# Optimization experiments

Hardware: AMD Instinct MI355X
Metric: run time of the kernel (lower is better)

The kernel has to match this reference:

```python
import jax, jax.numpy as jnp
import numpy as np
import math

N = 8192
D = 512

def setup_inputs() -> dict:
    key = jax.random.key(0)
    k1, k2, k3, k4, k5 = jax.random.split(key, 5)
    x = jax.random.normal(k1, (N, D), dtype=jnp.float32)
    mask = jax.random.randint(k2, (N, N), 0, 2) == 1
    s = 1.0 / math.sqrt(D)
    Wq = jax.random.normal(k3, (D, D), dtype=jnp.float32) * s
    Wk = jax.random.normal(k4, (D, D), dtype=jnp.float32) * s
    Wv = jax.random.normal(k5, (D, D), dtype=jnp.float32) * s
    return {"x": x, "mask": mask, "Wq": Wq, "Wk": Wk, "Wv": Wv}

def reference(x, mask, Wq, Wk, Wv):
    d_model = x.shape[-1]
    # torch nn.Linear: y = x @ W^T
    Q = x @ Wq.T
    K = x @ Wk.T
    V = x @ Wv.T
    scores = (Q @ K.T) / jnp.sqrt(jnp.asarray(d_model, x.dtype))  # [N, N]
    scores = jnp.where(mask, jnp.asarray(-1e9, x.dtype), scores)
    # manual stable softmax, matching the original op sequence
    scores = jnp.exp(scores - jnp.max(scores, axis=1, keepdims=True))
    attn = scores / jnp.sum(scores, axis=-1, keepdims=True)
    cntx = attn @ V
    return (cntx, attn)
```

## Files before the change

kernel.cpp:

```cpp
#include <hip/hip_runtime.h>

#define NTOK 8192
#define DMODEL 512

typedef _Float16 f16;
typedef _Float16 f16x4 __attribute__((ext_vector_type(4)));
typedef _Float16 f16x8 __attribute__((ext_vector_type(8)));
typedef float f32x4 __attribute__((ext_vector_type(4)));

__device__ __forceinline__ void async_ld16(const void* g, void* l) {
  __builtin_amdgcn_global_load_lds((const __attribute__((address_space(1))) void*)g,
                                   (__attribute__((address_space(3))) void*)l, 16, 0, 0);
}

__global__ void pack_f16(const float* __restrict__ s, f16* __restrict__ d, int n) {
  int i = (blockIdx.x * 256 + threadIdx.x) * 4;
  if (i >= n) return;
  float4 v = *(const float4*)(s + i);
  f16x4 h; h.x = (f16)v.x; h.y = (f16)v.y; h.z = (f16)v.z; h.w = (f16)v.w;
  *(f16x4*)(d + i) = h;
}

__global__ __launch_bounds__(256) void transpose_f16(const f16* __restrict__ src,
                                                     f16* __restrict__ dst) {
  __shared__ f16 T[64][72];
  int t = threadIdx.x;
  int tok0 = blockIdx.x * 64, d0 = blockIdx.y * 64;
#pragma unroll
  for (int i = 0; i < 2; ++i) {
    int row = (t >> 3) + i * 32;
    int col = (t & 7) * 8;
    f16x8 v = *(const f16x8*)(src + (size_t)(tok0 + row) * DMODEL + d0 + col);
    *(f16x8*)(&T[row][col]) = v;
  }
  __syncthreads();
#pragma unroll
  for (int i = 0; i < 2; ++i) {
    int od = (t >> 3) + i * 32;
    int ot = (t & 7) * 8;
    f16x8 v;
#pragma unroll
    for (int j = 0; j < 8; ++j) v[j] = T[ot + j][od];
    *(f16x8*)(dst + (size_t)(d0 + od) * NTOK + tok0 + ot) = v;
  }
}

__device__ __forceinline__ void stage128x32(const f16* G, int r0, int k0, int rs,
                                            f16* lds, int t) {
  int wv = t >> 6;
  const f16* g0 = G + (size_t)(r0 + (t >> 2)) * rs + k0 + (t & 3) * 8;
  async_ld16(g0, (char*)lds + wv * 1024);
  const f16* g1 = g0 + (size_t)64 * rs;
  async_ld16(g1, (char*)lds + 4096 + wv * 1024);
}

__global__ __launch_bounds__(256) void qkv_gemm(const f16* __restrict__ X,
                                                const f16* __restrict__ Wall,
                                                f16* __restrict__ Out) {
  __shared__ f16 As[128 * 32];
  __shared__ f16 Bs[128 * 32];
  int t = threadIdx.x;
  int z = blockIdx.z;
  const f16* B = Wall + (size_t)z * DMODEL * DMODEL;
  f16* C = Out + (size_t)z * NTOK * DMODEL;
  int m0 = blockIdx.y * 128, n0 = blockIdx.x * 128;
  int lane = t & 63, wv = t >> 6, quad = lane >> 4, l15 = lane & 15;
  int m_off = (wv & 1) * 64, n_off = (wv >> 1) * 64;
  f32x4 acc[4][4] = {};
  for (int kt = 0; kt < DMODEL; kt += 32) {
    __syncthreads();
    stage128x32(X, m0, kt, DMODEL, As, t);
    stage128x32(B, n0, kt, DMODEL, Bs, t);
    __syncthreads();
    f16x8 af[4], bf[4];
    const f16x8* Av = (const f16x8*)As;
    const f16x8* Bv = (const f16x8*)Bs;
#pragma unroll
    for (int mt = 0; mt < 4; ++mt) af[mt] = Av[(m_off + mt * 16 + l15) * 4 + quad];
#pragma unroll
    for (int nt = 0; nt < 4; ++nt) bf[nt] = Bv[(n_off + nt * 16 + l15) * 4 + quad];
#pragma unroll
    for (int mt = 0; mt < 4; ++mt)
#pragma unroll
      for (int nt = 0; nt < 4; ++nt)
        acc[mt][nt] = __builtin_amdgcn_mfma_f32_16x16x32_f16(af[mt], bf[nt], acc[mt][nt], 0, 0, 0);
  }
#pragma unroll
  for (int mt = 0; mt < 4; ++mt)
#pragma unroll
    for (int nt = 0; nt < 4; ++nt)
#pragma unroll
      for (int r = 0; r < 4; ++r) {
        int row = m0 + m_off + mt * 16 + quad * 4 + r;
        int col = n0 + n_off + nt * 16 + l15;
        C[(size_t)row * DMODEL + col] = (f16)acc[mt][nt][r];
      }
}

__global__ __launch_bounds__(256) void scores_kernel(const f16* __restrict__ Q,
                                                     const f16* __restrict__ Kh,
                                                     const int* __restrict__ mask,
                                                     float* __restrict__ E,
                                                     float* __restrict__ rowsum) {
  __shared__ f16 As[128 * 32];
  __shared__ f16 Bs[128 * 32];
  int t = threadIdx.x;
  int m0 = blockIdx.y * 128, n0 = blockIdx.x * 128;
  int lane = t & 63, wv = t >> 6, quad = lane >> 4, l15 = lane & 15;
  int m_off = (wv & 1) * 64, n_off = (wv >> 1) * 64;
  f32x4 acc[4][4] = {};
  for (int kt = 0; kt < DMODEL; kt += 32) {
    __syncthreads();
    stage128x32(Q, m0, kt, DMODEL, As, t);
    stage128x32(Kh, n0, kt, DMODEL, Bs, t);
    __syncthreads();
    f16x8 af[4], bf[4];
    const f16x8* Av = (const f16x8*)As;
    const f16x8* Bv = (const f16x8*)Bs;
#pragma unroll
    for (int mt = 0; mt < 4; ++mt) af[mt] = Av[(m_off + mt * 16 + l15) * 4 + quad];
#pragma unroll
    for (int nt = 0; nt < 4; ++nt) bf[nt] = Bv[(n_off + nt * 16 + l15) * 4 + quad];
#pragma unroll
    for (int mt = 0; mt < 4; ++mt)
#pragma unroll
      for (int nt = 0; nt < 4; ++nt)
        acc[mt][nt] = __builtin_amdgcn_mfma_f32_16x16x32_f16(af[mt], bf[nt], acc[mt][nt], 0, 0, 0);
  }
  const float scale = 0.044194173824159216f;
#pragma unroll
  for (int mt = 0; mt < 4; ++mt)
#pragma unroll
    for (int r = 0; r < 4; ++r) {
      int row = m0 + m_off + mt * 16 + quad * 4 + r;
      float rs = 0.f;
#pragma unroll
      for (int nt = 0; nt < 4; ++nt) {
        int col = n0 + n_off + nt * 16 + l15;
        size_t idx = (size_t)row * NTOK + col;
        float s = acc[mt][nt][r] * scale;
        float e = mask[idx] ? 0.f : __expf(s);
        E[idx] = e;
        rs += e;
      }
      rs += __shfl_xor(rs, 1);
      rs += __shfl_xor(rs, 2);
      rs += __shfl_xor(rs, 4);
      rs += __shfl_xor(rs, 8);
      if (l15 == 0) atomicAdd(&rowsum[row], rs);
    }
}

__global__ __launch_bounds__(512, 2) void norm_ev(float* __restrict__ E,
                                                  const float* __restrict__ rowsum,
                                                  const f16* __restrict__ Vt,
                                                  float* __restrict__ cntx) {
  __shared__ f16 Es[128 * 32];
  __shared__ f16 Vs[512 * 32];
  int t = threadIdx.x;
  int r0 = blockIdx.x * 128;
  int k0 = blockIdx.y * 2048;
  int lane = t & 63, wv = t >> 6, quad = lane >> 4, l15 = lane & 15;
  int m_off = (wv & 1) * 64, n_off = (wv >> 1) * 128;
  int srow = t >> 3, scol = (t & 7) * 4;
  float rinv0 = 1.f / rowsum[r0 + srow];
  float rinv1 = 1.f / rowsum[r0 + srow + 64];
  f32x4 acc[4][8] = {};
  for (int kt = k0; kt < k0 + 2048; kt += 32) {
    __syncthreads();
    {
      size_t g = (size_t)(r0 + srow) * NTOK + kt + scol;
      float4 v = *(const float4*)(E + g);
      v.x *= rinv0; v.y *= rinv0; v.z *= rinv0; v.w *= rinv0;
      *(float4*)(E + g) = v;
      f16x4 h; h.x = (f16)v.x; h.y = (f16)v.y; h.z = (f16)v.z; h.w = (f16)v.w;
      *(f16x4*)(Es + srow * 32 + scol) = h;
      size_t g2 = g + (size_t)64 * NTOK;
      float4 v2 = *(const float4*)(E + g2);
      v2.x *= rinv1; v2.y *= rinv1; v2.z *= rinv1; v2.w *= rinv1;
      *(float4*)(E + g2) = v2;
      f16x4 h2; h2.x = (f16)v2.x; h2.y = (f16)v2.y; h2.z = (f16)v2.z; h2.w = (f16)v2.w;
      *(f16x4*)(Es + (srow + 64) * 32 + scol) = h2;
    }
#pragma unroll
    for (int i = 0; i < 4; ++i) {
      const f16* g = Vt + (size_t)((i * 512 + t) >> 2) * NTOK + kt + (t & 3) * 8;
      async_ld16(g, (char*)Vs + i * 8192 + wv * 1024);
    }
    __syncthreads();
    f16x8 af[4], bf[8];
    const f16x8* Ev = (const f16x8*)Es;
    const f16x8* Vv = (const f16x8*)Vs;
#pragma unroll
    for (int mt = 0; mt < 4; ++mt) af[mt] = Ev[(m_off + mt * 16 + l15) * 4 + quad];
#pragma unroll
    for (int nt = 0; nt < 8; ++nt) bf[nt] = Vv[(n_off + nt * 16 + l15) * 4 + quad];
#pragma unroll
    for (int mt = 0; mt < 4; ++mt)
#pragma unroll
      for (int nt = 0; nt < 8; ++nt)
        acc[mt][nt] = __builtin_amdgcn_mfma_f32_16x16x32_f16(af[mt], bf[nt], acc[mt][nt], 0, 0, 0);
  }
#pragma unroll
  for (int mt = 0; mt < 4; ++mt)
#pragma unroll
    for (int nt = 0; nt < 8; ++nt)
#pragma unroll
      for (int r = 0; r < 4; ++r) {
        int row = r0 + m_off + mt * 16 + quad * 4 + r;
        int col = n_off + nt * 16 + l15;
        atomicAdd(&cntx[(size_t)row * DMODEL + col], acc[mt][nt][r]);
      }
}

extern "C" void kernel_launch(void* const* d_in, const int* in_sizes, int n_in,
                              void* d_out, int out_size, void* d_ws, size_t ws_size,
                              hipStream_t stream) {
  const float* x  = (const float*)d_in[0];
  const int* mask = (const int*)d_in[1];
  const float* Wq = (const float*)d_in[2];
  const float* Wk = (const float*)d_in[3];
  const float* Wv = (const float*)d_in[4];
  float* cntx = (float*)d_out;
  float* attn = (float*)d_out + (size_t)NTOK * DMODEL;

  f16* xh = (f16*)d_ws;
  f16* Wh = xh + (size_t)NTOK * DMODEL;
  f16* QKV = Wh + (size_t)3 * DMODEL * DMODEL;
  f16* Qh = QKV;
  f16* Kh = QKV + (size_t)NTOK * DMODEL;
  f16* Vh = QKV + (size_t)2 * NTOK * DMODEL;
  f16* Vt = QKV + (size_t)3 * NTOK * DMODEL;
  float* rowsum = (float*)(Vt + (size_t)NTOK * DMODEL);

  hipMemsetAsync(cntx, 0, (size_t)NTOK * DMODEL * sizeof(float), stream);
  hipMemsetAsync(rowsum, 0, NTOK * sizeof(float), stream);

  pack_f16<<<dim3(NTOK * DMODEL / 1024), 256, 0, stream>>>(x, xh, NTOK * DMODEL);
  pack_f16<<<dim3(DMODEL * DMODEL / 1024), 256, 0, stream>>>(Wq, Wh, DMODEL * DMODEL);
  pack_f16<<<dim3(DMODEL * DMODEL / 1024), 256, 0, stream>>>(Wk, Wh + DMODEL * DMODEL, DMODEL * DMODEL);
  pack_f16<<<dim3(DMODEL * DMODEL / 1024), 256, 0, stream>>>(Wv, Wh + 2 * DMODEL * DMODEL, DMODEL * DMODEL);

  qkv_gemm<<<dim3(DMODEL / 128, NTOK / 128, 3), 256, 0, stream>>>(xh, Wh, QKV);
  transpose_f16<<<dim3(NTOK / 64, DMODEL / 64), 256, 0, stream>>>(Vh, Vt);
  scores_kernel<<<dim3(NTOK / 128, NTOK / 128), 256, 0, stream>>>(Qh, Kh, mask, attn, rowsum);
  norm_ev<<<dim3(NTOK / 128, 4), 512, 0, stream>>>(attn, rowsum, Vt, cntx);
}
```

Baseline: 791.2 us.

## Bit-pack mask, store fp16 exp scores in-place, defer normalization to epilogues

Packs the int mask into 64-bit ballot words, which replaces the 256MB int read in the scores kernel. The scores kernel now writes unnormalized fp16 exponentials through a swizzled LDS tile into the attn buffer, using a 2x row stride. The PV kernel loads those fp16 values asynchronously and applies 1/rowsum in its epilogue, so it no longer does the fp32 read-modify-write of attn. A final in-place expand kernel converts the fp16 values back to normalized fp32 attn by walking backwards. The GEMM K-step also goes from 32 to 64. The cntx output buffer serves as scratch for the mask bits, and the attn values pass through fp16, which costs precision.

```diff
diff --git a/kernel.cpp b/kernel.cpp
--- a/kernel.cpp
+++ b/kernel.cpp
@@ -2,11 +2,14 @@
 
 #define NTOK 8192
 #define DMODEL 512
+#define NWORDS 128
+#define ESTRIDE (2 * NTOK)
 
 typedef _Float16 f16;
 typedef _Float16 f16x4 __attribute__((ext_vector_type(4)));
 typedef _Float16 f16x8 __attribute__((ext_vector_type(8)));
 typedef float f32x4 __attribute__((ext_vector_type(4)));
+typedef unsigned long long u64;
 
 __device__ __forceinline__ void async_ld16(const void* g, void* l) {
   __builtin_amdgcn_global_load_lds((const __attribute__((address_space(1))) void*)g,
@@ -21,6 +24,19 @@
   *(f16x4*)(d + i) = h;
 }
 
+__global__ __launch_bounds__(256) void pack_mask(const int* __restrict__ mask,
+                                                 u64* __restrict__ bits) {
+  int wave = (blockIdx.x * 256 + threadIdx.x) >> 6;
+  int lane = threadIdx.x & 63;
+  size_t W0 = (size_t)wave * 8;
+#pragma unroll
+  for (int i = 0; i < 8; ++i) {
+    int m = mask[(W0 + i) * 64 + lane];
+    u64 b = __ballot(m != 0);
+    if (lane == 0) bits[W0 + i] = b;
+  }
+}
+
 __global__ __launch_bounds__(256) void transpose_f16(const f16* __restrict__ src,
                                                      f16* __restrict__ dst) {
   __shared__ f16 T[64][72];
@@ -45,20 +61,48 @@
   }
 }
 
-__device__ __forceinline__ void stage128x32(const f16* G, int r0, int k0, int rs,
+__device__ __forceinline__ void stage128x64(const f16* G, int r0, int k0, int rs,
                                             f16* lds, int t) {
   int wv = t >> 6;
-  const f16* g0 = G + (size_t)(r0 + (t >> 2)) * rs + k0 + (t & 3) * 8;
-  async_ld16(g0, (char*)lds + wv * 1024);
-  const f16* g1 = g0 + (size_t)64 * rs;
-  async_ld16(g1, (char*)lds + 4096 + wv * 1024);
+  const f16* g = G + (size_t)(r0 + (t >> 3)) * rs + k0 + (t & 7) * 8;
+#pragma unroll
+  for (int i = 0; i < 4; ++i)
+    async_ld16(g + (size_t)i * 32 * rs, (char*)lds + i * 4096 + wv * 1024);
+}
+
+template <int RS>
+__device__ __forceinline__ void gemm128(const f16* A, const f16* B, int m0, int n0,
+                                        f16* As, f16* Bs, int t, f32x4 (&acc)[4][4]) {
+  int lane = t & 63, wv = t >> 6, quad = lane >> 4, l15 = lane & 15;
+  int m_off = (wv & 1) * 64, n_off = (wv >> 1) * 64;
+  for (int kt = 0; kt < RS; kt += 64) {
+    __syncthreads();
+    stage128x64(A, m0, kt, RS, As, t);
+    stage128x64(B, n0, kt, RS, Bs, t);
+    __syncthreads();
+#pragma unroll
+    for (int ks = 0; ks < 2; ++ks) {
+      f16x8 af[4], bf[4];
+#pragma unroll
+      for (int mt = 0; mt < 4; ++mt)
+        af[mt] = *(const f16x8*)(As + (m_off + mt * 16 + l15) * 64 + ks * 32 + quad * 8);
+#pragma unroll
+      for (int nt = 0; nt < 4; ++nt)
+        bf[nt] = *(const f16x8*)(Bs + (n_off + nt * 16 + l15) * 64 + ks * 32 + quad * 8);
+#pragma unroll
+      for (int mt = 0; mt < 4; ++mt)
+#pragma unroll
+        for (int nt = 0; nt < 4; ++nt)
+          acc[mt][nt] = __builtin_amdgcn_mfma_f32_16x16x32_f16(af[mt], bf[nt], acc[mt][nt], 0, 0, 0);
+    }
+  }
 }
 
 __global__ __launch_bounds__(256) void qkv_gemm(const f16* __restrict__ X,
                                                 const f16* __restrict__ Wall,
                                                 f16* __restrict__ Out) {
-  __shared__ f16 As[128 * 32];
-  __shared__ f16 Bs[128 * 32];
+  __shared__ f16 As[128 * 64];
+  __shared__ f16 Bs[128 * 64];
   int t = threadIdx.x;
   int z = blockIdx.z;
   const f16* B = Wall + (size_t)z * DMODEL * DMODEL;
@@ -67,24 +111,7 @@
   int lane = t & 63, wv = t >> 6, quad = lane >> 4, l15 = lane & 15;
   int m_off = (wv & 1) * 64, n_off = (wv >> 1) * 64;
   f32x4 acc[4][4] = {};
-  for (int kt = 0; kt < DMODEL; kt += 32) {
-    __syncthreads();
-    stage128x32(X, m0, kt, DMODEL, As, t);
-    stage128x32(B, n0, kt, DMODEL, Bs, t);
-    __syncthreads();
-    f16x8 af[4], bf[4];
-    const f16x8* Av = (const f16x8*)As;
-    const f16x8* Bv = (const f16x8*)Bs;
-#pragma unroll
-    for (int mt = 0; mt < 4; ++mt) af[mt] = Av[(m_off + mt * 16 + l15) * 4 + quad];
-#pragma unroll
-    for (int nt = 0; nt < 4; ++nt) bf[nt] = Bv[(n_off + nt * 16 + l15) * 4 + quad];
-#pragma unroll
-    for (int mt = 0; mt < 4; ++mt)
-#pragma unroll
-      for (int nt = 0; nt < 4; ++nt)
-        acc[mt][nt] = __builtin_amdgcn_mfma_f32_16x16x32_f16(af[mt], bf[nt], acc[mt][nt], 0, 0, 0);
-  }
+  gemm128<DMODEL>(X, B, m0, n0, As, Bs, t, acc);
 #pragma unroll
   for (int mt = 0; mt < 4; ++mt)
 #pragma unroll
@@ -97,51 +124,38 @@
       }
 }
 
-__global__ __launch_bounds__(256) void scores_kernel(const f16* __restrict__ Q,
-                                                     const f16* __restrict__ Kh,
-                                                     const int* __restrict__ mask,
-                                                     float* __restrict__ E,
-                                                     float* __restrict__ rowsum) {
-  __shared__ f16 As[128 * 32];
-  __shared__ f16 Bs[128 * 32];
+__global__ __launch_bounds__(256) void scores2(const f16* __restrict__ Q,
+                                               const f16* __restrict__ Kh,
+                                               const u64* __restrict__ bits,
+                                               f16* __restrict__ Eh,
+                                               float* __restrict__ rowsum) {
+  __shared__ f16 SM[128 * 128];
+  f16* As = SM;
+  f16* Bs = SM + 128 * 64;
   int t = threadIdx.x;
   int m0 = blockIdx.y * 128, n0 = blockIdx.x * 128;
   int lane = t & 63, wv = t >> 6, quad = lane >> 4, l15 = lane & 15;
   int m_off = (wv & 1) * 64, n_off = (wv >> 1) * 64;
   f32x4 acc[4][4] = {};
-  for (int kt = 0; kt < DMODEL; kt += 32) {
-    __syncthreads();
-    stage128x32(Q, m0, kt, DMODEL, As, t);
-    stage128x32(Kh, n0, kt, DMODEL, Bs, t);
-    __syncthreads();
-    f16x8 af[4], bf[4];
-    const f16x8* Av = (const f16x8*)As;
-    const f16x8* Bv = (const f16x8*)Bs;
-#pragma unroll
-    for (int mt = 0; mt < 4; ++mt) af[mt] = Av[(m_off + mt * 16 + l15) * 4 + quad];
-#pragma unroll
-    for (int nt = 0; nt < 4; ++nt) bf[nt] = Bv[(n_off + nt * 16 + l15) * 4 + quad];
-#pragma unroll
-    for (int mt = 0; mt < 4; ++mt)
-#pragma unroll
-      for (int nt = 0; nt < 4; ++nt)
-        acc[mt][nt] = __builtin_amdgcn_mfma_f32_16x16x32_f16(af[mt], bf[nt], acc[mt][nt], 0, 0, 0);
-  }
+  gemm128<DMODEL>(Q, Kh, m0, n0, As, Bs, t, acc);
   const float scale = 0.044194173824159216f;
+  __syncthreads();
 #pragma unroll
   for (int mt = 0; mt < 4; ++mt)
 #pragma unroll
     for (int r = 0; r < 4; ++r) {
-      int row = m0 + m_off + mt * 16 + quad * 4 + r;
+      int lrow = m_off + mt * 16 + quad * 4 + r;
+      int row = m0 + lrow;
+      u64 w = bits[(size_t)row * NWORDS + ((n0 + n_off) >> 6)];
       float rs = 0.f;
 #pragma unroll
       for (int nt = 0; nt < 4; ++nt) {
-        int col = n0 + n_off + nt * 16 + l15;
-        size_t idx = (size_t)row * NTOK + col;
         float s = acc[mt][nt][r] * scale;
-        float e = mask[idx] ? 0.f : __expf(s);
-        E[idx] = e;
+        float e = ((w >> (nt * 16 + l15)) & 1) ? 0.f : __expf(s);
         rs += e;
+        int col = n_off + nt * 16 + l15;
+        int phys = (((col >> 3) ^ (lrow & 15)) << 3) | (col & 7);
+        SM[lrow * 128 + phys] = (f16)e;
       }
       rs += __shfl_xor(rs, 1);
       rs += __shfl_xor(rs, 2);
@@ -149,12 +163,20 @@
       rs += __shfl_xor(rs, 8);
       if (l15 == 0) atomicAdd(&rowsum[row], rs);
     }
-}
-
-__global__ __launch_bounds__(512, 2) void norm_ev(float* __restrict__ E,
-                                                  const float* __restrict__ rowsum,
-                                                  const f16* __restrict__ Vt,
-                                                  float* __restrict__ cntx) {
+  __syncthreads();
+#pragma unroll
+  for (int p = 0; p < 8; ++p) {
+    int lrow = p * 16 + (t >> 4);
+    int cb = t & 15;
+    f16x8 v = *(const f16x8*)(SM + lrow * 128 + ((cb ^ (lrow & 15)) << 3));
+    *(f16x8*)(Eh + (size_t)(m0 + lrow) * ESTRIDE + n0 + cb * 8) = v;
+  }
+}
+
+__global__ __launch_bounds__(512, 2) void pv_kernel(const f16* __restrict__ Eh,
+                                                    const float* __restrict__ rowsum,
+                                                    const f16* __restrict__ Vt,
+                                                    float* __restrict__ cntx) {
   __shared__ f16 Es[128 * 32];
   __shared__ f16 Vs[512 * 32];
   int t = threadIdx.x;
@@ -162,39 +184,23 @@
   int k0 = blockIdx.y * 2048;
   int lane = t & 63, wv = t >> 6, quad = lane >> 4, l15 = lane & 15;
   int m_off = (wv & 1) * 64, n_off = (wv >> 1) * 128;
-  int srow = t >> 3, scol = (t & 7) * 4;
-  float rinv0 = 1.f / rowsum[r0 + srow];
-  float rinv1 = 1.f / rowsum[r0 + srow + 64];
   f32x4 acc[4][8] = {};
   for (int kt = k0; kt < k0 + 2048; kt += 32) {
     __syncthreads();
-    {
-      size_t g = (size_t)(r0 + srow) * NTOK + kt + scol;
-      float4 v = *(const float4*)(E + g);
-      v.x *= rinv0; v.y *= rinv0; v.z *= rinv0; v.w *= rinv0;
-      *(float4*)(E + g) = v;
-      f16x4 h; h.x = (f16)v.x; h.y = (f16)v.y; h.z = (f16)v.z; h.w = (f16)v.w;
-      *(f16x4*)(Es + srow * 32 + scol) = h;
-      size_t g2 = g + (size_t)64 * NTOK;
-      float4 v2 = *(const float4*)(E + g2);
-      v2.x *= rinv1; v2.y *= rinv1; v2.z *= rinv1; v2.w *= rinv1;
-      *(float4*)(E + g2) = v2;
-      f16x4 h2; h2.x = (f16)v2.x; h2.y = (f16)v2.y; h2.z = (f16)v2.z; h2.w = (f16)v2.w;
-      *(f16x4*)(Es + (srow + 64) * 32 + scol) = h2;
-    }
-#pragma unroll
-    for (int i = 0; i < 4; ++i) {
-      const f16* g = Vt + (size_t)((i * 512 + t) >> 2) * NTOK + kt + (t & 3) * 8;
-      async_ld16(g, (char*)Vs + i * 8192 + wv * 1024);
-    }
+    async_ld16(Eh + (size_t)(r0 + (t >> 2)) * ESTRIDE + kt + (t & 3) * 8,
+               (char*)Es + wv * 1024);
+#pragma unroll
+    for (int i = 0; i < 4; ++i)
+      async_ld16(Vt + (size_t)((i * 512 + t) >> 2) * NTOK + kt + (t & 3) * 8,
+                 (char*)Vs + i * 8192 + wv * 1024);
     __syncthreads();
     f16x8 af[4], bf[8];
-    const f16x8* Ev = (const f16x8*)Es;
-    const f16x8* Vv = (const f16x8*)Vs;
-#pragma unroll
-    for (int mt = 0; mt < 4; ++mt) af[mt] = Ev[(m_off + mt * 16 + l15) * 4 + quad];
-#pragma unroll
-    for (int nt = 0; nt < 8; ++nt) bf[nt] = Vv[(n_off + nt * 16 + l15) * 4 + quad];
+#pragma unroll
+    for (int mt = 0; mt < 4; ++mt)
+      af[mt] = *(const f16x8*)(Es + (m_off + mt * 16 + l15) * 32 + quad * 8);
+#pragma unroll
+    for (int nt = 0; nt < 8; ++nt)
+      bf[nt] = *(const f16x8*)(Vs + (n_off + nt * 16 + l15) * 32 + quad * 8);
 #pragma unroll
     for (int mt = 0; mt < 4; ++mt)
 #pragma unroll
@@ -204,13 +210,36 @@
 #pragma unroll
   for (int mt = 0; mt < 4; ++mt)
 #pragma unroll
-    for (int nt = 0; nt < 8; ++nt)
-#pragma unroll
-      for (int r = 0; r < 4; ++r) {
-        int row = r0 + m_off + mt * 16 + quad * 4 + r;
+    for (int r = 0; r < 4; ++r) {
+      int row = r0 + m_off + mt * 16 + quad * 4 + r;
+      float ri = 1.0f / rowsum[row];
+#pragma unroll
+      for (int nt = 0; nt < 8; ++nt) {
         int col = n_off + nt * 16 + l15;
-        atomicAdd(&cntx[(size_t)row * DMODEL + col], acc[mt][nt][r]);
+        atomicAdd(&cntx[(size_t)row * DMODEL + col], acc[mt][nt][r] * ri);
       }
+    }
+}
+
+__global__ __launch_bounds__(256) void expand_attn(float* __restrict__ attn,
+                                                   const float* __restrict__ rowsum) {
+  int t = threadIdx.x;
+  int row = blockIdx.x * 4 + (t >> 6);
+  size_t rb = (size_t)row * NTOK;
+  const f16* Ehrow = (const f16*)(attn + rb);
+  float ri = 1.0f / rowsum[row];
+  int c0 = (t & 63) * 8;
+  for (int c = NTOK - 512; c >= 0; c -= 512) {
+    f16x8 v = *(const f16x8*)(Ehrow + c + c0);
+    __syncthreads();
+    float4 lo, hi;
+    lo.x = (float)v[0] * ri; lo.y = (float)v[1] * ri;
+    lo.z = (float)v[2] * ri; lo.w = (float)v[3] * ri;
+    hi.x = (float)v[4] * ri; hi.y = (float)v[5] * ri;
+    hi.z = (float)v[6] * ri; hi.w = (float)v[7] * ri;
+    *(float4*)(attn + rb + c + c0) = lo;
+    *(float4*)(attn + rb + c + c0 + 4) = hi;
+  }
 }
 
 extern "C" void kernel_launch(void* const* d_in, const int* in_sizes, int n_in,
@@ -233,16 +262,22 @@
   f16* Vt = QKV + (size_t)3 * NTOK * DMODEL;
   float* rowsum = (float*)(Vt + (size_t)NTOK * DMODEL);
 
-  hipMemsetAsync(cntx, 0, (size_t)NTOK * DMODEL * sizeof(float), stream);
+  u64* bits = (u64*)cntx;
+  f16* Eh = (f16*)attn;
+
   hipMemsetAsync(rowsum, 0, NTOK * sizeof(float), stream);
 
   pack_f16<<<dim3(NTOK * DMODEL / 1024), 256, 0, stream>>>(x, xh, NTOK * DMODEL);
   pack_f16<<<dim3(DMODEL * DMODEL / 1024), 256, 0, stream>>>(Wq, Wh, DMODEL * DMODEL);
   pack_f16<<<dim3(DMODEL * DMODEL / 1024), 256, 0, stream>>>(Wk, Wh + DMODEL * DMODEL, DMODEL * DMODEL);
   pack_f16<<<dim3(DMODEL * DMODEL / 1024), 256, 0, stream>>>(Wv, Wh + 2 * DMODEL * DMODEL, DMODEL * DMODEL);
+  pack_mask<<<dim3(NTOK * NWORDS / 8 / 4), 256, 0, stream>>>(mask, bits);
 
   qkv_gemm<<<dim3(DMODEL / 128, NTOK / 128, 3), 256, 0, stream>>>(xh, Wh, QKV);
   transpose_f16<<<dim3(NTOK / 64, DMODEL / 64), 256, 0, stream>>>(Vh, Vt);
-  scores_kernel<<<dim3(NTOK / 128, NTOK / 128), 256, 0, stream>>>(Qh, Kh, mask, attn, rowsum);
-  norm_ev<<<dim3(NTOK / 128, 4), 512, 0, stream>>>(attn, rowsum, Vt, cntx);
-}
+  scores2<<<dim3(NTOK / 128, NTOK / 128), 256, 0, stream>>>(Qh, Kh, bits, Eh, rowsum);
+
+  hipMemsetAsync(cntx, 0, (size_t)NTOK * DMODEL * sizeof(float), stream);
+  pv_kernel<<<dim3(NTOK / 128, 4), 512, 0, stream>>>(Eh, rowsum, Vt, cntx);
+  expand_attn<<<dim3(NTOK / 4), 256, 0, stream>>>(attn, rowsum);
+}
```

New measurement: 896.7 us. +13.3%, slower.
